# Performance work log

Measured on AMD Instinct MI355X. Metric: run time of the kernel, lower is better.

The kernel has to match this reference:

```python
import jax, jax.numpy as jnp
import numpy as np

N = 50000      # nodes
E = 800000     # edges
P = 200000     # link pairs
D_IN = 128     # input_dim
F_NUM = 128    # filter_num
OUT = 2        # out_dim
K = 10         # APPNP propagation steps
ALPHA = 0.1    # teleport prob


def setup_inputs() -> dict:
    key = jax.random.key(0)
    ks = jax.random.split(key, 9)
    x = jax.random.normal(ks[0], (N, D_IN), dtype=jnp.float32)
    edge_index = jax.random.randint(ks[1], (2, E), 0, N)
    index = jax.random.randint(ks[2], (P, 2), 0, N)
    s1 = 1.0 / np.sqrt(D_IN)
    s2 = 1.0 / np.sqrt(F_NUM)
    s3 = 1.0 / np.sqrt(2 * F_NUM)
    W1 = jax.random.uniform(ks[3], (F_NUM, D_IN), minval=-s1, maxval=s1)
    b1 = jax.random.uniform(ks[4], (F_NUM,), minval=-s1, maxval=s1)
    W2 = jax.random.uniform(ks[5], (F_NUM, F_NUM), minval=-s2, maxval=s2)
    b2 = jax.random.uniform(ks[6], (F_NUM,), minval=-s2, maxval=s2)
    W3 = jax.random.uniform(ks[7], (OUT, 2 * F_NUM), minval=-s3, maxval=s3)
    b3 = jax.random.uniform(ks[8], (OUT,), minval=-s3, maxval=s3)
    return {"x": x, "edge_index": edge_index, "index": index,
            "W1": W1, "b1": b1, "W2": W2, "b2": b2, "W3": W3, "b3": b3}


def _gcn_norm(edge_index, num_nodes):
    # PyG gcn_norm: add self-loops, sym norm D^{-1/2} (A+I) D^{-1/2}
    src, dst = edge_index[0], edge_index[1]
    loop = jnp.arange(num_nodes, dtype=src.dtype)
    src = jnp.concatenate([src, loop])
    dst = jnp.concatenate([dst, loop])
    deg = jax.ops.segment_sum(jnp.ones_like(src, dtype=jnp.float32), dst,
                              num_segments=num_nodes)
    dinv = jnp.where(deg > 0, jax.lax.rsqrt(deg), 0.0)
    norm = dinv[src] * dinv[dst]  # [E+N]
    return src, dst, norm


def _appnp(x, src, dst, norm, num_nodes):
    # h_{k+1} = (1-alpha) * A_hat h_k + alpha * x0
    def step(h, _):
        agg = jax.ops.segment_sum(norm[:, None] * h[src], dst,
                                  num_segments=num_nodes)
        return (1.0 - ALPHA) * agg + ALPHA * x, None
    h, _ = jax.lax.scan(step, x, None, length=K)
    return h


def reference(x, edge_index, index, W1, b1, W2, b2, W3, b3):
    num_nodes = x.shape[0]
    src, dst, norm = _gcn_norm(edge_index, num_nodes)
    h = x @ W1.T + b1                      # [N, F]
    h = jax.nn.relu(_appnp(h, src, dst, norm, num_nodes))
    h = h @ W2.T + b2                      # [N, F]
    h = jax.nn.relu(_appnp(h, src, dst, norm, num_nodes))
    feat = jnp.concatenate([h[index[:, 0]], h[index[:, 1]]], axis=-1)  # [P, 2F]
    out = feat @ W3.T + b3                 # [P, OUT]
    return jax.nn.log_softmax(out, axis=1)
```

## Files before the change

### kernel.cpp

```cpp
#include <hip/hip_runtime.h>
#include <math.h>

#define NN 50000
#define NE 800000
#define NP 200000
#define NF 128
#define NNP (NN + 1)
#define NEDGE_TOT (NE + NN)
#define NBLK 196
#define NBK 64
#define DPB 782
#define BKCAP 16384
#define EPB 2048
#define NSL 2
#define SF 64
#define NCPAD 1000064

typedef __attribute__((ext_vector_type(8))) short short8;
typedef __attribute__((ext_vector_type(4))) float float4v;
typedef __attribute__((ext_vector_type(2))) _Float16 h2;
typedef __attribute__((ext_vector_type(4))) unsigned short us4;

__device__ __forceinline__ unsigned short f2bf(float f) {
    unsigned u = __float_as_uint(f);
    return (unsigned short)((u + 0x7fffu + ((u >> 16) & 1u)) >> 16);
}
__device__ __forceinline__ unsigned pack2bf(float a, float b) {
    return (unsigned)f2bf(a) | ((unsigned)f2bf(b) << 16);
}

__device__ __forceinline__ h2 u2h2(unsigned u) {
    union { unsigned u; h2 h; } c; c.u = u; return c.h;
}
__device__ __forceinline__ unsigned h22u(h2 h) {
    union { unsigned u; h2 h; } c; c.h = h; return c.u;
}
__device__ __forceinline__ float h_lo(unsigned u) { return (float)u2h2(u).x; }
__device__ __forceinline__ float h_hi(unsigned u) { return (float)u2h2(u).y; }
__device__ __forceinline__ unsigned pack2h(float a, float b) {
    h2 h; h.x = (_Float16)a; h.y = (_Float16)b; return h22u(h);
}

__global__ __launch_bounds__(256) void init_cnt_k(int* __restrict__ cnt,
                                                  float4* __restrict__ puv) {
    int i = blockIdx.x * 256 + threadIdx.x;
    if (i < NN) {
        cnt[i] = 1;
        puv[i] = make_float4(0.f, 0.f, 0.f, 0.f);
    }
}

__global__ __launch_bounds__(256) void count_k(const int* __restrict__ ei,
                                               int* __restrict__ cnt) {
    int e = blockIdx.x * 256 + threadIdx.x;
    if (e < NE) atomicAdd(&cnt[ei[NE + e]], 1);
}

__global__ __launch_bounds__(256) void scan_reduce_k(const int* __restrict__ cnt,
                                                     int* __restrict__ bsum,
                                                     float* __restrict__ dinv) {
    __shared__ int s[256];
    int t = threadIdx.x;
    int idx = blockIdx.x * 256 + t;
    int v = (idx < NN) ? cnt[idx] : 0;
    if (idx < NN) dinv[idx] = rsqrtf((float)v);
    int vp = (v + 3) & ~3;
    s[t] = vp;
    __syncthreads();
    for (int off = 128; off > 0; off >>= 1) {
        if (t < off) s[t] += s[t + off];
        __syncthreads();
    }
    if (t == 0) bsum[blockIdx.x] = s[0];
}

__global__ __launch_bounds__(256) void scan_bsums_k(const int* __restrict__ bsum,
                                                    int* __restrict__ boff) {
    __shared__ int s[256];
    int t = threadIdx.x;
    int v = (t < NBLK) ? bsum[t] : 0;
    s[t] = v;
    __syncthreads();
    for (int off = 1; off < 256; off <<= 1) {
        int add = (t >= off) ? s[t - off] : 0;
        __syncthreads();
        s[t] += add;
        __syncthreads();
    }
    if (t < NBLK) boff[t] = s[t] - v;
}

__global__ __launch_bounds__(256) void scan_down_k(const int* __restrict__ cnt,
                                                   const int* __restrict__ boff,
                                                   int* __restrict__ row_ptr) {
    __shared__ int s[256];
    int t = threadIdx.x;
    int idx = blockIdx.x * 256 + t;
    int v = (idx < NN) ? ((cnt[idx] + 3) & ~3) : 0;
    s[t] = v;
    __syncthreads();
    for (int off = 1; off < 256; off <<= 1) {
        int add = (t >= off) ? s[t - off] : 0;
        __syncthreads();
        s[t] += add;
        __syncthreads();
    }
    int excl = s[t] - v + boff[blockIdx.x] + 4;
    if (idx < NN) {
        row_ptr[idx] = excl;
        if (idx == NN - 1) row_ptr[NN] = excl + v;
    }
}

__global__ __launch_bounds__(256) void fill_cols_k(unsigned* __restrict__ colsu) {
    int t = blockIdx.x * 256 + threadIdx.x;
    if (t < NCPAD / 2) colsu[t] = (unsigned)NN | ((unsigned)NN << 16);
}

__global__ __launch_bounds__(256) void bin_k(const int* __restrict__ ei,
                                             int* __restrict__ gtail,
                                             int2* __restrict__ gbk) {
    __shared__ int cntA[NBK], baseA[NBK], gposA[NBK];
    __shared__ int2 stage[EPB];
    int tid = threadIdx.x;
    int ebase = blockIdx.x * EPB;
    int sv[8], dv[8], lp8[8], bk8[8];
    bool val[8];
    if (tid < NBK) cntA[tid] = 0;
    __syncthreads();
#pragma unroll
    for (int k = 0; k < 8; ++k) {
        int e = ebase + k * 256 + tid;
        val[k] = (e < NEDGE_TOT);
        if (val[k]) {
            int s, d;
            if (e < NE) { s = ei[e]; d = ei[NE + e]; }
            else        { s = d = e - NE; }
            sv[k] = s; dv[k] = d;
            bk8[k] = d / DPB;
            lp8[k] = atomicAdd(&cntA[bk8[k]], 1);
        }
    }
    __syncthreads();
    if (tid == 0) {
        int run = 0;
        for (int b = 0; b < NBK; ++b) { baseA[b] = run; run += cntA[b]; }
    }
    __syncthreads();
    if (tid < NBK && cntA[tid] > 0)
        gposA[tid] = atomicAdd(&gtail[tid], cntA[tid]);
    __syncthreads();
#pragma unroll
    for (int k = 0; k < 8; ++k)
        if (val[k]) {
            int2 r; r.x = sv[k]; r.y = dv[k];
            stage[baseA[bk8[k]] + lp8[k]] = r;
        }
    __syncthreads();
    int total = baseA[NBK - 1] + cntA[NBK - 1];
    for (int i = tid; i < total; i += 256) {
        int2 r = stage[i];
        int b = r.y / DPB;
        gbk[(size_t)b * BKCAP + gposA[b] + (i - baseA[b])] = r;
    }
}

__global__ __launch_bounds__(256) void build_k(const int* __restrict__ row_ptr,
                                               const int* __restrict__ gtail,
                                               const int2* __restrict__ gbk,
                                               unsigned short* __restrict__ cols) {
    __shared__ int wcur[DPB];
    int tid = threadIdx.x;
    int b = blockIdx.x;
    int d0 = b * DPB;
    for (int i = tid; i < DPB; i += 256) {
        int d = d0 + i;
        wcur[i] = (d < NN) ? row_ptr[d] : 0;
    }
    __syncthreads();
    int nb = gtail[b];
    const int2* src = gbk + (size_t)b * BKCAP;
    for (int t = tid; t < nb; t += 256) {
        int2 r = src[t];
        int pos = atomicAdd(&wcur[r.y - d0], 1);
        cols[pos] = (unsigned short)r.x;
    }
}

__global__ __launch_bounds__(256) void zero_k(unsigned short* Ys1, unsigned short* Ys2,
                                              unsigned short* HA, unsigned short* HB,
                                              int* gtail) {
    int t = threadIdx.x;
    unsigned short* bufs[4] = {Ys1, Ys2, HA, HB};
    unsigned short* bp = bufs[t >> 6];
    int s = (t >> 5) & 1, u = t & 31;
    ((unsigned*)(bp + ((size_t)s * NNP + NN) * SF))[u] = 0u;
    if (t < NBK) gtail[t] = 0;
}

__global__ __launch_bounds__(256) void cast_w_k(const float* __restrict__ W,
                                                unsigned short* __restrict__ Wb) {
    int t = blockIdx.x * 256 + threadIdx.x;
    if (t >= 128 * 128 / 8) return;
    int i = t * 8;
    float4 f0 = *(const float4*)(W + i);
    float4 f1 = *(const float4*)(W + i + 4);
    uint4 q;
    q.x = pack2bf(f0.x, f0.y);
    q.y = pack2bf(f0.z, f0.w);
    q.z = pack2bf(f1.x, f1.y);
    q.w = pack2bf(f1.z, f1.w);
    *(uint4*)(Wb + i) = q;
}

#define GPAD 136
template <bool F32IN>
__global__ __launch_bounds__(256) void gemm_mfma_k(const void* __restrict__ Xv,
                                                   const unsigned short* __restrict__ Wb,
                                                   const float* __restrict__ bias,
                                                   const float* __restrict__ dinv,
                                                   unsigned short* __restrict__ Yu,
                                                   unsigned short* __restrict__ Ys,
                                                   int nrows) {
    __shared__ unsigned short sm[4 * 16 * GPAD];
    int wave = threadIdx.x >> 6, lane = threadIdx.x & 63;
    int rbase = blockIdx.x * 64 + wave * 16;
    if (rbase >= nrows) return;
    int quad = lane >> 4, mn = lane & 15;
    float4v acc[8];
#pragma unroll
    for (int ft = 0; ft < 8; ++ft) acc[ft] = (float4v){0.f, 0.f, 0.f, 0.f};
#pragma unroll
    for (int kb = 0; kb < 128; kb += 32) {
        short8 a;
        if (F32IN) {
            const float* X = (const float*)Xv;
            float4 f0 = *(const float4*)(X + (size_t)(rbase + mn) * NF + kb + quad * 8);
            float4 f1 = *(const float4*)(X + (size_t)(rbase + mn) * NF + kb + quad * 8 + 4);
            a[0] = (short)f2bf(f0.x); a[1] = (short)f2bf(f0.y);
            a[2] = (short)f2bf(f0.z); a[3] = (short)f2bf(f0.w);
            a[4] = (short)f2bf(f1.x); a[5] = (short)f2bf(f1.y);
            a[6] = (short)f2bf(f1.z); a[7] = (short)f2bf(f1.w);
        } else {
            const unsigned short* X = (const unsigned short*)Xv;
            a = *(const short8*)(X + (size_t)(rbase + mn) * NF + kb + quad * 8);
        }
#pragma unroll
        for (int ft = 0; ft < 8; ++ft) {
            short8 b = *(const short8*)(Wb + (size_t)(ft * 16 + mn) * NF + kb + quad * 8);
            acc[ft] = __builtin_amdgcn_mfma_f32_16x16x32_bf16(a, b, acc[ft], 0, 0, 0);
        }
    }
    unsigned short* smw = sm + wave * 16 * GPAD;
#pragma unroll
    for (int ft = 0; ft < 8; ++ft) {
        float bv = bias[ft * 16 + mn];
#pragma unroll
        for (int r = 0; r < 4; ++r) {
            union { _Float16 h; unsigned short s; } cv;
            cv.h = (_Float16)(acc[ft][r] + bv);
            smw[(quad * 4 + r) * GPAD + ft * 16 + mn] = cv.s;
        }
    }
    __syncthreads();
#pragma unroll
    for (int t = 0; t < 4; ++t) {
        int rl = t * 4 + quad;
        int row = rbase + rl;
        uint4 q = *(const uint4*)(smw + rl * GPAD + mn * 8);
        size_t sb = ((size_t)(mn >> 3) * NNP + row) * SF + (mn & 7) * 8;
        *(uint4*)(Yu + sb) = q;
        float g = dinv[row];
        uint4 qs;
        qs.x = pack2h(g * h_lo(q.x), g * h_hi(q.x));
        qs.y = pack2h(g * h_lo(q.y), g * h_hi(q.y));
        qs.z = pack2h(g * h_lo(q.z), g * h_hi(q.z));
        qs.w = pack2h(g * h_lo(q.w), g * h_hi(q.w));
        *(uint4*)(Ys + sb) = qs;
    }
}

__global__ __launch_bounds__(512) void appnp_slice_k(
    const unsigned short* __restrict__ hs,
    const unsigned short* __restrict__ x0,
    const float* __restrict__ dinv,
    unsigned short* __restrict__ out,
    const int* __restrict__ row_ptr,
    const unsigned short* __restrict__ cols,
    int mode,
    const float* __restrict__ W3,
    float* __restrict__ puv) {
    int b = blockIdx.x;
    int s = b & 1;
    int wave = threadIdx.x >> 6, lane = threadIdx.x & 63;
    int g = lane >> 3, fo = lane & 7;
    int wid = (b >> 1) * 64 + wave * 8 + g;
    bool valid = wid < NN;
    int nid = valid ? wid : NN;
    const unsigned short* hsS = hs + (size_t)s * NNP * SF;
    int beg = 0, dp = 0;
    if (valid) { beg = row_ptr[wid]; dp = row_ptr[wid + 1] - beg; }
    int dpm = dp;
    dpm = max(dpm, __shfl_xor(dpm, 8, 64));
    dpm = max(dpm, __shfl_xor(dpm, 16, 64));
    dpm = max(dpm, __shfl_xor(dpm, 32, 64));
    float gsc = valid ? dinv[wid] : 0.f;
    uint4 xq = *(const uint4*)(x0 + ((size_t)s * NNP + nid) * SF + fo * 8);
    h2 a01; a01.x = (_Float16)0.f; a01.y = (_Float16)0.f;
    h2 a23 = a01, a45 = a01, a67 = a01;
    if (dpm > 0) {
        int fb8 = fo * 8;
        auto colsat = [&](int j4) -> us4 {
            int o = (j4 < dp) ? beg + j4 : 0;
            return __builtin_nontemporal_load((const us4*)(cols + o));
        };
        us4 c0 = colsat(0);
        us4 c1 = colsat(4);
        us4 c2 = colsat(8);
        uint4 A0 = *(const uint4*)(hsS + (size_t)c0.x * SF + fb8);
        uint4 A1 = *(const uint4*)(hsS + (size_t)c0.y * SF + fb8);
        uint4 A2 = *(const uint4*)(hsS + (size_t)c0.z * SF + fb8);
        uint4 A3 = *(const uint4*)(hsS + (size_t)c0.w * SF + fb8);
        uint4 B0 = *(const uint4*)(hsS + (size_t)c1.x * SF + fb8);
        uint4 B1 = *(const uint4*)(hsS + (size_t)c1.y * SF + fb8);
        uint4 B2 = *(const uint4*)(hsS + (size_t)c1.z * SF + fb8);
        uint4 B3 = *(const uint4*)(hsS + (size_t)c1.w * SF + fb8);
        for (int j = 0; j < dpm; j += 4) {
            us4 c3 = colsat(j + 12);
            uint4 C0 = *(const uint4*)(hsS + (size_t)c2.x * SF + fb8);
            uint4 C1 = *(const uint4*)(hsS + (size_t)c2.y * SF + fb8);
            uint4 C2 = *(const uint4*)(hsS + (size_t)c2.z * SF + fb8);
            uint4 C3 = *(const uint4*)(hsS + (size_t)c2.w * SF + fb8);
            a01 += (u2h2(A0.x) + u2h2(A1.x)) + (u2h2(A2.x) + u2h2(A3.x));
            a23 += (u2h2(A0.y) + u2h2(A1.y)) + (u2h2(A2.y) + u2h2(A3.y));
            a45 += (u2h2(A0.z) + u2h2(A1.z)) + (u2h2(A2.z) + u2h2(A3.z));
            a67 += (u2h2(A0.w) + u2h2(A1.w)) + (u2h2(A2.w) + u2h2(A3.w));
            A0 = B0; A1 = B1; A2 = B2; A3 = B3;
            B0 = C0; B1 = C1; B2 = C2; B3 = C3;
            c2 = c3;
        }
    }
    float s9 = 0.9f * gsc;
    float h0 = s9 * (float)a01.x + 0.1f * h_lo(xq.x);
    float h1 = s9 * (float)a01.y + 0.1f * h_hi(xq.x);
    float h2v = s9 * (float)a23.x + 0.1f * h_lo(xq.y);
    float h3 = s9 * (float)a23.y + 0.1f * h_hi(xq.y);
    float h4 = s9 * (float)a45.x + 0.1f * h_lo(xq.z);
    float h5 = s9 * (float)a45.y + 0.1f * h_hi(xq.z);
    float h6 = s9 * (float)a67.x + 0.1f * h_lo(xq.w);
    float h7 = s9 * (float)a67.y + 0.1f * h_hi(xq.w);
    if (mode == 0) {
        if (valid) {
            uint4 oq;
            oq.x = pack2h(gsc * h0, gsc * h1);
            oq.y = pack2h(gsc * h2v, gsc * h3);
            oq.z = pack2h(gsc * h4, gsc * h5);
            oq.w = pack2h(gsc * h6, gsc * h7);
            *(uint4*)(out + ((size_t)s * NNP + wid) * SF + fo * 8) = oq;
        }
    } else {
        h0 = fmaxf(h0, 0.f); h1 = fmaxf(h1, 0.f);
        h2v = fmaxf(h2v, 0.f); h3 = fmaxf(h3, 0.f);
        h4 = fmaxf(h4, 0.f); h5 = fmaxf(h5, 0.f);
        h6 = fmaxf(h6, 0.f); h7 = fmaxf(h7, 0.f);
        if (mode == 1) {
            if (valid) {
                uint4 oq;
                oq.x = pack2bf(h0, h1);
                oq.y = pack2bf(h2v, h3);
                oq.z = pack2bf(h4, h5);
                oq.w = pack2bf(h6, h7);
                *(uint4*)(out + (size_t)wid * NF + s * SF + fo * 8) = oq;
            }
        } else {
            int fb = s * SF + fo * 8;
            float4 wu0a = *(const float4*)(W3 + fb);
            float4 wu0b = *(const float4*)(W3 + fb + 4);
            float4 wv0a = *(const float4*)(W3 + 128 + fb);
            float4 wv0b = *(const float4*)(W3 + 128 + fb + 4);
            float4 wu1a = *(const float4*)(W3 + 256 + fb);
            float4 wu1b = *(const float4*)(W3 + 256 + fb + 4);
            float4 wv1a = *(const float4*)(W3 + 384 + fb);
            float4 wv1b = *(const float4*)(W3 + 384 + fb + 4);
            float du0 = h0 * wu0a.x + h1 * wu0a.y + h2v * wu0a.z + h3 * wu0a.w
                      + h4 * wu0b.x + h5 * wu0b.y + h6 * wu0b.z + h7 * wu0b.w;
            float du1 = h0 * wu1a.x + h1 * wu1a.y + h2v * wu1a.z + h3 * wu1a.w
                      + h4 * wu1b.x + h5 * wu1b.y + h6 * wu1b.z + h7 * wu1b.w;
            float dv0 = h0 * wv0a.x + h1 * wv0a.y + h2v * wv0a.z + h3 * wv0a.w
                      + h4 * wv0b.x + h5 * wv0b.y + h6 * wv0b.z + h7 * wv0b.w;
            float dv1 = h0 * wv1a.x + h1 * wv1a.y + h2v * wv1a.z + h3 * wv1a.w
                      + h4 * wv1b.x + h5 * wv1b.y + h6 * wv1b.z + h7 * wv1b.w;
            du0 += __shfl_xor(du0, 1, 64); du0 += __shfl_xor(du0, 2, 64);
            du0 += __shfl_xor(du0, 4, 64);
            du1 += __shfl_xor(du1, 1, 64); du1 += __shfl_xor(du1, 2, 64);
            du1 += __shfl_xor(du1, 4, 64);
            dv0 += __shfl_xor(dv0, 1, 64); dv0 += __shfl_xor(dv0, 2, 64);
            dv0 += __shfl_xor(dv0, 4, 64);
            dv1 += __shfl_xor(dv1, 1, 64); dv1 += __shfl_xor(dv1, 2, 64);
            dv1 += __shfl_xor(dv1, 4, 64);
            if (valid && fo < 4) {
                float v = (fo == 0) ? du0 : (fo == 1) ? du1
                          : (fo == 2) ? dv0 : dv1;
                atomicAdd(&puv[(size_t)wid * 4 + fo], v);
            }
        }
    }
}

__global__ __launch_bounds__(256) void pair2_k(const float4* __restrict__ puv,
                                               const int2* __restrict__ index,
                                               const float* __restrict__ b3,
                                               float* __restrict__ outp) {
    int p = blockIdx.x * 256 + threadIdx.x;
    if (p >= NP) return;
    int2 uv = index[p];
    float4 a = puv[uv.x];
    float4 b = puv[uv.y];
    float s0 = a.x + b.z + b3[0];
    float s1 = a.y + b.w + b3[1];
    float m = fmaxf(s0, s1);
    float lse = m + logf(expf(s0 - m) + expf(s1 - m));
    *(float2*)(outp + (size_t)p * 2) = make_float2(s0 - lse, s1 - lse);
}

extern "C" void kernel_launch(void* const* d_in, const int* in_sizes, int n_in,
                              void* d_out, int out_size, void* d_ws, size_t ws_size,
                              hipStream_t stream) {
    const float* x  = (const float*)d_in[0];
    const int* ei   = (const int*)d_in[1];
    const int* idx  = (const int*)d_in[2];
    const float* W1 = (const float*)d_in[3];
    const float* b1 = (const float*)d_in[4];
    const float* W2 = (const float*)d_in[5];
    const float* b2 = (const float*)d_in[6];
    const float* W3 = (const float*)d_in[7];
    const float* b3 = (const float*)d_in[8];
    float* out = (float*)d_out;

    char* ws = (char*)d_ws;
    size_t off = 0;
    auto alloc = [&](size_t bytes) -> void* {
        void* p = ws + off;
        off = (off + bytes + 255) & ~(size_t)255;
        return p;
    };
    const size_t HROWS = (size_t)NSL * NNP * SF;
    int*   cnt     = (int*)  alloc(NN * sizeof(int));
    float* dinv    = (float*)alloc(NN * sizeof(float));
    int*   row_ptr = (int*)  alloc((NN + 1) * sizeof(int));
    int*   bsum    = (int*)  alloc(NBLK * sizeof(int));
    int*   boff    = (int*)  alloc(NBLK * sizeof(int));
    int*   gtail   = (int*)  alloc(NBK * sizeof(int));
    int2*  gbk     = (int2*) alloc((size_t)NBK * BKCAP * sizeof(int2));
    unsigned short* cols = (unsigned short*)alloc((size_t)NCPAD * 2);
    float4* puv    = (float4*)alloc((size_t)NN * sizeof(float4));
    unsigned short* Wb1 = (unsigned short*)alloc(128 * 128 * 2);
    unsigned short* Wb2 = (unsigned short*)alloc(128 * 128 * 2);
    unsigned short* Yu1 = (unsigned short*)alloc(HROWS * 2);
    unsigned short* Ys1 = (unsigned short*)alloc(HROWS * 2);
    unsigned short* Yu2 = (unsigned short*)alloc(HROWS * 2);
    unsigned short* Ys2 = (unsigned short*)alloc(HROWS * 2);
    unsigned short* HA  = (unsigned short*)alloc(HROWS * 2);
    unsigned short* HB  = (unsigned short*)alloc(HROWS * 2);
    unsigned short* Hrelu = (unsigned short*)alloc((size_t)NN * NF * 2);

    const int gN    = (NN + 255) / 256;
    const int gE    = (NE + 255) / 256;
    const int gBin  = (NEDGE_TOT + EPB - 1) / EPB;
    const int gGemm = (NN + 63) / 64;
    const int gFill = (NCPAD / 2 + 255) / 256;
    const int gSlice = ((NN + 63) / 64) * 2;
    const int gPair = (NP + 255) / 256;

    cast_w_k<<<8, 256, 0, stream>>>(W1, Wb1);
    cast_w_k<<<8, 256, 0, stream>>>(W2, Wb2);
    zero_k<<<1, 256, 0, stream>>>(Ys1, Ys2, HA, HB, gtail);
    init_cnt_k<<<gN, 256, 0, stream>>>(cnt, puv);
    count_k<<<gE, 256, 0, stream>>>(ei, cnt);
    scan_reduce_k<<<NBLK, 256, 0, stream>>>(cnt, bsum, dinv);
    scan_bsums_k<<<1, 256, 0, stream>>>(bsum, boff);
    scan_down_k<<<NBLK, 256, 0, stream>>>(cnt, boff, row_ptr);
    fill_cols_k<<<gFill, 256, 0, stream>>>((unsigned*)cols);
    bin_k<<<gBin, 256, 0, stream>>>(ei, gtail, gbk);
    build_k<<<NBK, 256, 0, stream>>>(row_ptr, gtail, gbk, cols);

    float* puvf = (float*)puv;
    gemm_mfma_k<true><<<gGemm, 256, 0, stream>>>(x, Wb1, b1, dinv, Yu1, Ys1, NN);
    {
        const unsigned short* cur = Ys1;
        for (int k = 0; k < 10; ++k) {
            unsigned short* dst = (k == 9) ? Hrelu : ((k & 1) ? HB : HA);
            appnp_slice_k<<<gSlice, 512, 0, stream>>>(cur, Yu1, dinv, dst, row_ptr,
                                                      cols, (k == 9) ? 1 : 0, W3, puvf);
            cur = dst;
        }
    }
    gemm_mfma_k<false><<<gGemm, 256, 0, stream>>>(Hrelu, Wb2, b2, dinv, Yu2, Ys2, NN);
    {
        const unsigned short* cur = Ys2;
        for (int k = 0; k < 10; ++k) {
            unsigned short* dst = (k & 1) ? HB : HA;
            appnp_slice_k<<<gSlice, 512, 0, stream>>>(cur, Yu2, dinv, dst, row_ptr,
                                                      cols, (k == 9) ? 2 : 0, W3, puvf);
            cur = dst;
        }
    }
    pair2_k<<<gPair, 256, 0, stream>>>(puv, (const int2*)idx, b3, out);
}
```

Before: 754.7 us.

## Handle self-loops inline and deepen gather prefetch in APPNP slice kernel

Self-loop edges are no longer stored in the CSR column list. Each node's own row is loaded directly and added to the aggregate, which shrinks the padded rows and the binning work. The gather loop's software pipeline grows from three to four groups of four neighbours in flight. Loads of x0 and stores of the relu output now use nontemporal hints. Deeper prefetch raises register pressure, and the padding now rounds (cnt+2) down to a multiple of four, which assumes cnt includes the self-loop and must stay consistent with build_k.

```diff
diff --git a/kernel.cpp b/kernel.cpp
--- a/kernel.cpp
+++ b/kernel.cpp
@@ -6,7 +6,6 @@
 #define NP 200000
 #define NF 128
 #define NNP (NN + 1)
-#define NEDGE_TOT (NE + NN)
 #define NBLK 196
 #define NBK 64
 #define DPB 782
@@ -20,6 +19,7 @@
 typedef __attribute__((ext_vector_type(4))) float float4v;
 typedef __attribute__((ext_vector_type(2))) _Float16 h2;
 typedef __attribute__((ext_vector_type(4))) unsigned short us4;
+typedef __attribute__((ext_vector_type(4))) unsigned int u32x4;
 
 __device__ __forceinline__ unsigned short f2bf(float f) {
     unsigned u = __float_as_uint(f);
@@ -64,7 +64,7 @@
     int idx = blockIdx.x * 256 + t;
     int v = (idx < NN) ? cnt[idx] : 0;
     if (idx < NN) dinv[idx] = rsqrtf((float)v);
-    int vp = (v + 3) & ~3;
+    int vp = (idx < NN) ? ((v + 2) & ~3) : 0;
     s[t] = vp;
     __syncthreads();
     for (int off = 128; off > 0; off >>= 1) {
@@ -96,7 +96,7 @@
     __shared__ int s[256];
     int t = threadIdx.x;
     int idx = blockIdx.x * 256 + t;
-    int v = (idx < NN) ? ((cnt[idx] + 3) & ~3) : 0;
+    int v = (idx < NN) ? ((cnt[idx] + 2) & ~3) : 0;
     s[t] = v;
     __syncthreads();
     for (int off = 1; off < 256; off <<= 1) {
@@ -131,11 +131,9 @@
 #pragma unroll
     for (int k = 0; k < 8; ++k) {
         int e = ebase + k * 256 + tid;
-        val[k] = (e < NEDGE_TOT);
+        val[k] = (e < NE);
         if (val[k]) {
-            int s, d;
-            if (e < NE) { s = ei[e]; d = ei[NE + e]; }
-            else        { s = d = e - NE; }
+            int s = ei[e], d = ei[NE + e];
             sv[k] = s; dv[k] = d;
             bk8[k] = d / DPB;
             lp8[k] = atomicAdd(&cntA[bk8[k]], 1);
@@ -298,6 +296,7 @@
     bool valid = wid < NN;
     int nid = valid ? wid : NN;
     const unsigned short* hsS = hs + (size_t)s * NNP * SF;
+    int fb8 = fo * 8;
     int beg = 0, dp = 0;
     if (valid) { beg = row_ptr[wid]; dp = row_ptr[wid + 1] - beg; }
     int dpm = dp;
@@ -305,41 +304,43 @@
     dpm = max(dpm, __shfl_xor(dpm, 16, 64));
     dpm = max(dpm, __shfl_xor(dpm, 32, 64));
     float gsc = valid ? dinv[wid] : 0.f;
-    uint4 xq = *(const uint4*)(x0 + ((size_t)s * NNP + nid) * SF + fo * 8);
+    u32x4 xq = __builtin_nontemporal_load(
+        (const u32x4*)(x0 + ((size_t)s * NNP + nid) * SF + fb8));
+    uint4 own = *(const uint4*)(hsS + (size_t)nid * SF + fb8);
     h2 a01; a01.x = (_Float16)0.f; a01.y = (_Float16)0.f;
     h2 a23 = a01, a45 = a01, a67 = a01;
     if (dpm > 0) {
-        int fb8 = fo * 8;
         auto colsat = [&](int j4) -> us4 {
             int o = (j4 < dp) ? beg + j4 : 0;
             return __builtin_nontemporal_load((const us4*)(cols + o));
         };
-        us4 c0 = colsat(0);
-        us4 c1 = colsat(4);
-        us4 c2 = colsat(8);
-        uint4 A0 = *(const uint4*)(hsS + (size_t)c0.x * SF + fb8);
-        uint4 A1 = *(const uint4*)(hsS + (size_t)c0.y * SF + fb8);
-        uint4 A2 = *(const uint4*)(hsS + (size_t)c0.z * SF + fb8);
-        uint4 A3 = *(const uint4*)(hsS + (size_t)c0.w * SF + fb8);
-        uint4 B0 = *(const uint4*)(hsS + (size_t)c1.x * SF + fb8);
-        uint4 B1 = *(const uint4*)(hsS + (size_t)c1.y * SF + fb8);
-        uint4 B2 = *(const uint4*)(hsS + (size_t)c1.z * SF + fb8);
-        uint4 B3 = *(const uint4*)(hsS + (size_t)c1.w * SF + fb8);
+        auto gat = [&](unsigned short c) -> uint4 {
+            return *(const uint4*)(hsS + (size_t)c * SF + fb8);
+        };
+        us4 cq0 = colsat(0);
+        us4 cq1 = colsat(4);
+        us4 cq2 = colsat(8);
+        us4 cq3 = colsat(12);
+        uint4 A0 = gat(cq0.x), A1 = gat(cq0.y), A2 = gat(cq0.z), A3 = gat(cq0.w);
+        uint4 B0 = gat(cq1.x), B1 = gat(cq1.y), B2 = gat(cq1.z), B3 = gat(cq1.w);
+        uint4 C0 = gat(cq2.x), C1 = gat(cq2.y), C2 = gat(cq2.z), C3 = gat(cq2.w);
         for (int j = 0; j < dpm; j += 4) {
-            us4 c3 = colsat(j + 12);
-            uint4 C0 = *(const uint4*)(hsS + (size_t)c2.x * SF + fb8);
-            uint4 C1 = *(const uint4*)(hsS + (size_t)c2.y * SF + fb8);
-            uint4 C2 = *(const uint4*)(hsS + (size_t)c2.z * SF + fb8);
-            uint4 C3 = *(const uint4*)(hsS + (size_t)c2.w * SF + fb8);
+            us4 cq4 = colsat(j + 16);
+            uint4 D0 = gat(cq3.x), D1 = gat(cq3.y), D2 = gat(cq3.z), D3 = gat(cq3.w);
             a01 += (u2h2(A0.x) + u2h2(A1.x)) + (u2h2(A2.x) + u2h2(A3.x));
             a23 += (u2h2(A0.y) + u2h2(A1.y)) + (u2h2(A2.y) + u2h2(A3.y));
             a45 += (u2h2(A0.z) + u2h2(A1.z)) + (u2h2(A2.z) + u2h2(A3.z));
             a67 += (u2h2(A0.w) + u2h2(A1.w)) + (u2h2(A2.w) + u2h2(A3.w));
             A0 = B0; A1 = B1; A2 = B2; A3 = B3;
             B0 = C0; B1 = C1; B2 = C2; B3 = C3;
-            c2 = c3;
-        }
-    }
+            C0 = D0; C1 = D1; C2 = D2; C3 = D3;
+            cq3 = cq4;
+        }
+    }
+    a01 += u2h2(own.x);
+    a23 += u2h2(own.y);
+    a45 += u2h2(own.z);
+    a67 += u2h2(own.w);
     float s9 = 0.9f * gsc;
     float h0 = s9 * (float)a01.x + 0.1f * h_lo(xq.x);
     float h1 = s9 * (float)a01.y + 0.1f * h_hi(xq.x);
@@ -356,7 +357,7 @@
             oq.y = pack2h(gsc * h2v, gsc * h3);
             oq.z = pack2h(gsc * h4, gsc * h5);
             oq.w = pack2h(gsc * h6, gsc * h7);
-            *(uint4*)(out + ((size_t)s * NNP + wid) * SF + fo * 8) = oq;
+            *(uint4*)(out + ((size_t)s * NNP + wid) * SF + fb8) = oq;
         }
     } else {
         h0 = fmaxf(h0, 0.f); h1 = fmaxf(h1, 0.f);
@@ -365,15 +366,16 @@
         h6 = fmaxf(h6, 0.f); h7 = fmaxf(h7, 0.f);
         if (mode == 1) {
             if (valid) {
-                uint4 oq;
+                u32x4 oq;
                 oq.x = pack2bf(h0, h1);
                 oq.y = pack2bf(h2v, h3);
                 oq.z = pack2bf(h4, h5);
                 oq.w = pack2bf(h6, h7);
-                *(uint4*)(out + (size_t)wid * NF + s * SF + fo * 8) = oq;
+                __builtin_nontemporal_store(
+                    oq, (u32x4*)(out + (size_t)wid * NF + s * SF + fb8));
             }
         } else {
-            int fb = s * SF + fo * 8;
+            int fb = s * SF + fb8;
             float4 wu0a = *(const float4*)(W3 + fb);
             float4 wu0b = *(const float4*)(W3 + fb + 4);
             float4 wv0a = *(const float4*)(W3 + 128 + fb);
@@ -466,7 +468,7 @@
 
     const int gN    = (NN + 255) / 256;
     const int gE    = (NE + 255) / 256;
-    const int gBin  = (NEDGE_TOT + EPB - 1) / EPB;
+    const int gBin  = (NE + EPB - 1) / EPB;
     const int gGemm = (NN + 63) / 64;
     const int gFill = (NCPAD / 2 + 255) / 256;
     const int gSlice = ((NN + 63) / 64) * 2;
```

Measured after the change: 752.5 us, median of 2. Within noise of the previous version (-0.3%).
